# Kernel tuning notes

Hardware: AMD Instinct MI355X
Metric: run time of the kernel (lower is better)

## Reference

```python
import jax, jax.numpy as jnp
import numpy as np

B, T, IN_F, F = 128, 256, 256, 256
TAU_MEM = 0.02
THRESH = 0.5
RESET = 0.0
BETA = 4.0
LN_EPS = 1e-6

# Fast-sigmoid surrogate spike: forward = Heaviside, backward = 1/(1+beta|x|)^2
@jax.custom_vjp
def spike_surrogate(x):
    return (x > 0.0).astype(x.dtype)

def _sp_fwd(x):
    return spike_surrogate(x), x

def _sp_bwd(x, g):
    return (g / jnp.square(1.0 + BETA * jnp.abs(x)),)

spike_surrogate.defvjp(_sp_fwd, _sp_bwd)


def setup_inputs() -> dict:
    key = jax.random.key(0)
    k0, k1 = jax.random.split(key)
    spikes = jax.random.uniform(k0, (B, T, IN_F), dtype=jnp.float32)
    W = jax.random.normal(k1, (IN_F, F), dtype=jnp.float32) / np.sqrt(IN_F)
    b = jnp.zeros((F,), jnp.float32)
    ln_scale = jnp.ones((T, F), jnp.float32)   # distinct LayerNorm per timestep
    ln_bias = jnp.zeros((T, F), jnp.float32)
    return {"spikes": spikes, "W": W, "b": b, "ln_scale": ln_scale, "ln_bias": ln_bias}


def reference(spikes, W, b, ln_scale, ln_bias):
    # Dense is shared across timesteps -> one big contraction, same math.
    currents = jnp.einsum('bti,if->btf', spikes, W) + b  # [B,T,F]
    alpha = jnp.exp(jnp.asarray(-1.0 / TAU_MEM, spikes.dtype))

    def step(v_mem, xs):
        cur, gamma, beta_ln = xs  # [B,F], [F], [F]
        v_mem = alpha * v_mem + (1.0 - alpha) * cur
        s = spike_surrogate(v_mem - THRESH)
        v_mem = v_mem * (1.0 - s) + RESET * s
        mu = jnp.mean(s, axis=-1, keepdims=True)
        var = jnp.var(s, axis=-1, keepdims=True)
        y = (s - mu) * jax.lax.rsqrt(var + LN_EPS) * gamma + beta_ln
        return v_mem, y

    v0 = jnp.zeros((spikes.shape[0], W.shape[1]), spikes.dtype)
    xs = (jnp.swapaxes(currents, 0, 1), ln_scale, ln_bias)  # time-major
    _, ys = jax.lax.scan(step, v0, xs)  # ys: [T,B,F]
    return jnp.swapaxes(ys, 0, 1)  # [B,T,F]
```

## Files before the change

### kernel.cpp

```cpp
#include <hip/hip_runtime.h>
#include <math.h>

#define NROWS 32768
#define NK 256
#define NF 256
#define NT_SEQ 256
#define MTILE 32
#define TAU 8e-3f


typedef __attribute__((ext_vector_type(4))) float f32x4;
typedef __attribute__((ext_vector_type(8))) short bf16x8;

__device__ __forceinline__ unsigned short bf16_rne(float f) {
    unsigned int u = __builtin_bit_cast(unsigned int, f);
    u += 0x7FFFu + ((u >> 16) & 1u);
    return (unsigned short)(u >> 16);
}

__global__ void prep_w(const float* __restrict__ W,
                       unsigned short* __restrict__ wt,
                       float* __restrict__ wtT) {
    const int k = blockIdx.x;
    const int col = threadIdx.x;
    const float w = W[k * NF + col];
    const int ks = k >> 5, chunk = (k >> 3) & 3, j = k & 7;
    wt[(ks * 4 + chunk) * 2048 + col * 8 + j] = bf16_rne(w);
    wtT[col * NK + k] = w;
}

__global__ __launch_bounds__(512)
void lif_main(const float* __restrict__ spikes,
              const float* __restrict__ bias,
              const float* __restrict__ ln_scale,
              const float* __restrict__ ln_bias,
              const unsigned short* __restrict__ wt,
              const float* __restrict__ wtT,
              float* __restrict__ out)
{
    __shared__ __align__(16) short alds[MTILE][264];
    __shared__ unsigned int bits[MTILE][8];
    __shared__ float rinv_s[MTILE], mu_s[MTILE];
    __shared__ unsigned int elist[256];
    __shared__ int ecnt;

    const int tid = threadIdx.x;
    const int lane = tid & 63;
    const int wid = tid >> 6;
    const int row0 = blockIdx.x * MTILE;

    if (tid == 0) ecnt = 0;

    #pragma unroll
    for (int it = 0; it < 2; ++it) {
        const int idx = it * 512 + tid;
        const int r = idx >> 5, c8 = (idx & 31) * 8;
        const float* p = spikes + (size_t)(row0 + r) * NK + c8;
        const float4 u = *reinterpret_cast<const float4*>(p);
        const float4 v = *reinterpret_cast<const float4*>(p + 4);
        const unsigned int w0 = (unsigned int)bf16_rne(u.x) | ((unsigned int)bf16_rne(u.y) << 16);
        const unsigned int w1 = (unsigned int)bf16_rne(u.z) | ((unsigned int)bf16_rne(u.w) << 16);
        const unsigned int w2 = (unsigned int)bf16_rne(v.x) | ((unsigned int)bf16_rne(v.y) << 16);
        const unsigned int w3 = (unsigned int)bf16_rne(v.z) | ((unsigned int)bf16_rne(v.w) << 16);
        *reinterpret_cast<uint4*>(&alds[r][c8]) = make_uint4(w0, w1, w2, w3);
    }
    __syncthreads();

    f32x4 acc[2][2];
    {
        const f32x4 z = {0.f, 0.f, 0.f, 0.f};
        acc[0][0] = z; acc[0][1] = z; acc[1][0] = z; acc[1][1] = z;
    }
    const int a_off = (lane & 15) * 264 + (lane >> 4) * 8;
    const int b_base = (lane >> 4) * 2048 + (wid * 32 + (lane & 15)) * 8;
    const short* alds_flat = &alds[0][0];

    #pragma unroll
    for (int ks = 0; ks < 8; ++ks) {
        const bf16x8 b0 = *reinterpret_cast<const bf16x8*>(wt + ks * 8192 + b_base);
        const bf16x8 b1 = *reinterpret_cast<const bf16x8*>(wt + ks * 8192 + b_base + 128);
        const bf16x8 a0 = *reinterpret_cast<const bf16x8*>(alds_flat + ks * 32 + a_off);
        const bf16x8 a1 = *reinterpret_cast<const bf16x8*>(alds_flat + 16 * 264 + ks * 32 + a_off);
        acc[0][0] = __builtin_amdgcn_mfma_f32_16x16x32_bf16(a0, b0, acc[0][0], 0, 0, 0);
        acc[0][1] = __builtin_amdgcn_mfma_f32_16x16x32_bf16(a0, b1, acc[0][1], 0, 0, 0);
        acc[1][0] = __builtin_amdgcn_mfma_f32_16x16x32_bf16(a1, b0, acc[1][0], 0, 0, 0);
        acc[1][1] = __builtin_amdgcn_mfma_f32_16x16x32_bf16(a1, b1, acc[1][1], 0, 0, 0);
    }

    unsigned int smask[2] = {0u, 0u};
    #pragma unroll
    for (int mt = 0; mt < 2; ++mt)
        #pragma unroll
        for (int nt = 0; nt < 2; ++nt) {
            const int gcol = wid * 32 + nt * 16 + (lane & 15);
            const float bv = bias[gcol];
            #pragma unroll
            for (int reg = 0; reg < 4; ++reg) {
                const float v = acc[mt][nt][reg] + bv;
                if ((v - 0.5f) > 0.0f) smask[mt] |= 1u << (nt * 4 + reg);
                if (__builtin_expect(fabsf(v - 0.5f) < TAU, 0)) {
                    const int rl = mt * 16 + (lane >> 4) * 4 + reg;
                    const int ei = atomicAdd(&ecnt, 1);
                    if (ei < 256) elist[ei] = (unsigned int)((rl << 8) | gcol);
                }
            }
        }

    #pragma unroll
    for (int mt = 0; mt < 2; ++mt)
        #pragma unroll
        for (int reg = 0; reg < 4; ++reg) {
            const unsigned long long m0 = __ballot((smask[mt] >> (reg)) & 1u);
            const unsigned long long m1 = __ballot((smask[mt] >> (4 + reg)) & 1u);
            if (lane < 4) {
                const int g = lane;
                const unsigned int w =
                    (unsigned int)((m0 >> (g * 16)) & 0xFFFFull) |
                    ((unsigned int)((m1 >> (g * 16)) & 0xFFFFull) << 16);
                bits[mt * 16 + g * 4 + reg][wid] = w;
            }
        }
    __syncthreads();

    const int ne = min(ecnt, 256);
    for (int e = wid; e < ne; e += 8) {
        const unsigned int pk = elist[e];
        const int rl = (int)(pk >> 8), gcol = (int)(pk & 255u);
        const float* sr = spikes + (size_t)(row0 + rl) * NK;
        const float* wc = wtT + (size_t)gcol * NK;
        const int k0 = lane * 4;
        const float4 s4 = *reinterpret_cast<const float4*>(sr + k0);
        const float4 w4 = *reinterpret_cast<const float4*>(wc + k0);
        const double p0 = (double)s4.x * (double)w4.x;
        const double p1 = (double)s4.y * (double)w4.y;
        const double p2 = (double)s4.z * (double)w4.z;
        const double p3 = (double)s4.w * (double)w4.w;
        double pl = (p0 + p1) + (p2 + p3);
        #pragma unroll
        for (int off = 32; off > 0; off >>= 1) pl += __shfl_down(pl, off);
        if (lane == 0) {
            const double vex = pl + (double)bias[gcol];
            const bool sex = (vex - 0.5) > 0.0;
            const bool spv = (bits[rl][gcol >> 5] >> (gcol & 31)) & 1u;
            if (sex != spv) atomicXor(&bits[rl][gcol >> 5], 1u << (gcol & 31));
        }
    }
    __syncthreads();

    if (tid < MTILE) {
        int kc = 0;
        #pragma unroll
        for (int w = 0; w < 8; ++w) kc += __popc(bits[tid][w]);
        const double mu = (double)kc * (1.0 / 256.0);
        const double var = mu * (1.0 - mu);
        rinv_s[tid] = (float)(1.0 / sqrt(var + 1e-6));
        mu_s[tid] = (float)mu;
    }
    __syncthreads();

    const int orow = tid >> 4;
    const int of0 = (tid & 15) * 4;
    const int grow = row0 + orow;
    const int t = grow & (NT_SEQ - 1);
    const float rinv = rinv_s[orow];
    const float muf = mu_s[orow];
    #pragma unroll
    for (int j = 0; j < 4; ++j) {
        const int f = of0 + j * 64;
        const unsigned int wb = bits[orow][f >> 5];
        const int sh = f & 31;
        const float4 g4 = *reinterpret_cast<const float4*>(&ln_scale[t * NF + f]);
        const float4 b4 = *reinterpret_cast<const float4*>(&ln_bias[t * NF + f]);
        float4 o;
        const float s0 = ((wb >> (sh + 0)) & 1u) ? 1.0f : 0.0f;
        const float s1 = ((wb >> (sh + 1)) & 1u) ? 1.0f : 0.0f;
        const float s2 = ((wb >> (sh + 2)) & 1u) ? 1.0f : 0.0f;
        const float s3 = ((wb >> (sh + 3)) & 1u) ? 1.0f : 0.0f;
        o.x = (s0 - muf) * rinv * g4.x + b4.x;
        o.y = (s1 - muf) * rinv * g4.y + b4.y;
        o.z = (s2 - muf) * rinv * g4.z + b4.z;
        o.w = (s3 - muf) * rinv * g4.w + b4.w;
        *reinterpret_cast<float4*>(&out[(size_t)grow * NF + f]) = o;
    }
}

extern "C" void kernel_launch(void* const* d_in, const int* in_sizes, int n_in,
                              void* d_out, int out_size, void* d_ws, size_t ws_size,
                              hipStream_t stream) {
    const float* spikes   = (const float*)d_in[0];
    const float* W        = (const float*)d_in[1];
    const float* bias     = (const float*)d_in[2];
    const float* ln_scale = (const float*)d_in[3];
    const float* ln_bias  = (const float*)d_in[4];
    float* out = (float*)d_out;
    unsigned short* wt = (unsigned short*)d_ws;
    float* wtT = (float*)((char*)d_ws + 131072);

    prep_w<<<dim3(256), dim3(256), 0, stream>>>(W, wt, wtT);
    lif_main<<<dim3(NROWS / MTILE), dim3(512), 0, stream>>>(
        spikes, bias, ln_scale, ln_bias, wt, wtT, out);
}
```

Measured before the change: 39.61 us.

## Process two row tiles per block with prefetch of the second tile

Each block now handles two 32-row tiles, halving the grid. Global loads for the second tile are issued before the first tile's MFMA and epilogue, and the bf16 conversion into a second LDS buffer happens after the first tile's matmul. This is meant to hide global load latency behind compute and to amortize block launch and setup. The cost is fewer blocks in flight, more registers and LDS per block, and an extra sync between tiles.

```diff
diff --git a/kernel.cpp b/kernel.cpp
--- a/kernel.cpp
+++ b/kernel.cpp
@@ -38,7 +38,7 @@
               const float* __restrict__ wtT,
               float* __restrict__ out)
 {
-    __shared__ __align__(16) short alds[MTILE][264];
+    __shared__ __align__(16) short alds[2][MTILE][264];
     __shared__ unsigned int bits[MTILE][8];
     __shared__ float rinv_s[MTILE], mu_s[MTILE];
     __shared__ unsigned int elist[256];
@@ -47,140 +47,170 @@
     const int tid = threadIdx.x;
     const int lane = tid & 63;
     const int wid = tid >> 6;
-    const int row0 = blockIdx.x * MTILE;
+    const int row_base = blockIdx.x * (2 * MTILE);
 
     if (tid == 0) ecnt = 0;
 
-    #pragma unroll
-    for (int it = 0; it < 2; ++it) {
-        const int idx = it * 512 + tid;
-        const int r = idx >> 5, c8 = (idx & 31) * 8;
-        const float* p = spikes + (size_t)(row0 + r) * NK + c8;
-        const float4 u = *reinterpret_cast<const float4*>(p);
-        const float4 v = *reinterpret_cast<const float4*>(p + 4);
-        const unsigned int w0 = (unsigned int)bf16_rne(u.x) | ((unsigned int)bf16_rne(u.y) << 16);
-        const unsigned int w1 = (unsigned int)bf16_rne(u.z) | ((unsigned int)bf16_rne(u.w) << 16);
-        const unsigned int w2 = (unsigned int)bf16_rne(v.x) | ((unsigned int)bf16_rne(v.y) << 16);
-        const unsigned int w3 = (unsigned int)bf16_rne(v.z) | ((unsigned int)bf16_rne(v.w) << 16);
-        *reinterpret_cast<uint4*>(&alds[r][c8]) = make_uint4(w0, w1, w2, w3);
-    }
-    __syncthreads();
-
-    f32x4 acc[2][2];
-    {
-        const f32x4 z = {0.f, 0.f, 0.f, 0.f};
-        acc[0][0] = z; acc[0][1] = z; acc[1][0] = z; acc[1][1] = z;
-    }
+    const int r0 = tid >> 5, r1 = 16 + (tid >> 5), c8 = (tid & 31) * 8;
+
     const int a_off = (lane & 15) * 264 + (lane >> 4) * 8;
     const int b_base = (lane >> 4) * 2048 + (wid * 32 + (lane & 15)) * 8;
-    const short* alds_flat = &alds[0][0];
-
-    #pragma unroll
-    for (int ks = 0; ks < 8; ++ks) {
-        const bf16x8 b0 = *reinterpret_cast<const bf16x8*>(wt + ks * 8192 + b_base);
-        const bf16x8 b1 = *reinterpret_cast<const bf16x8*>(wt + ks * 8192 + b_base + 128);
-        const bf16x8 a0 = *reinterpret_cast<const bf16x8*>(alds_flat + ks * 32 + a_off);
-        const bf16x8 a1 = *reinterpret_cast<const bf16x8*>(alds_flat + 16 * 264 + ks * 32 + a_off);
-        acc[0][0] = __builtin_amdgcn_mfma_f32_16x16x32_bf16(a0, b0, acc[0][0], 0, 0, 0);
-        acc[0][1] = __builtin_amdgcn_mfma_f32_16x16x32_bf16(a0, b1, acc[0][1], 0, 0, 0);
-        acc[1][0] = __builtin_amdgcn_mfma_f32_16x16x32_bf16(a1, b0, acc[1][0], 0, 0, 0);
-        acc[1][1] = __builtin_amdgcn_mfma_f32_16x16x32_bf16(a1, b1, acc[1][1], 0, 0, 0);
+
+    auto cvt8 = [&](const float4& u, const float4& v) -> uint4 {
+        return make_uint4(
+            (unsigned int)bf16_rne(u.x) | ((unsigned int)bf16_rne(u.y) << 16),
+            (unsigned int)bf16_rne(u.z) | ((unsigned int)bf16_rne(u.w) << 16),
+            (unsigned int)bf16_rne(v.x) | ((unsigned int)bf16_rne(v.y) << 16),
+            (unsigned int)bf16_rne(v.z) | ((unsigned int)bf16_rne(v.w) << 16));
+    };
+
+    float4 u0, v0, u1, v1;
+    {
+        const float* p0 = spikes + (size_t)(row_base + r0) * NK + c8;
+        const float* p1 = spikes + (size_t)(row_base + r1) * NK + c8;
+        u0 = *reinterpret_cast<const float4*>(p0);
+        v0 = *reinterpret_cast<const float4*>(p0 + 4);
+        u1 = *reinterpret_cast<const float4*>(p1);
+        v1 = *reinterpret_cast<const float4*>(p1 + 4);
     }
-
-    unsigned int smask[2] = {0u, 0u};
-    #pragma unroll
-    for (int mt = 0; mt < 2; ++mt)
-        #pragma unroll
-        for (int nt = 0; nt < 2; ++nt) {
-            const int gcol = wid * 32 + nt * 16 + (lane & 15);
-            const float bv = bias[gcol];
-            #pragma unroll
-            for (int reg = 0; reg < 4; ++reg) {
-                const float v = acc[mt][nt][reg] + bv;
-                if ((v - 0.5f) > 0.0f) smask[mt] |= 1u << (nt * 4 + reg);
-                if (__builtin_expect(fabsf(v - 0.5f) < TAU, 0)) {
-                    const int rl = mt * 16 + (lane >> 4) * 4 + reg;
-                    const int ei = atomicAdd(&ecnt, 1);
-                    if (ei < 256) elist[ei] = (unsigned int)((rl << 8) | gcol);
+    *reinterpret_cast<uint4*>(&alds[0][r0][c8]) = cvt8(u0, v0);
+    *reinterpret_cast<uint4*>(&alds[0][r1][c8]) = cvt8(u1, v1);
+    __syncthreads();
+
+    {
+        const float* p0 = spikes + (size_t)(row_base + MTILE + r0) * NK + c8;
+        const float* p1 = spikes + (size_t)(row_base + MTILE + r1) * NK + c8;
+        u0 = *reinterpret_cast<const float4*>(p0);
+        v0 = *reinterpret_cast<const float4*>(p0 + 4);
+        u1 = *reinterpret_cast<const float4*>(p1);
+        v1 = *reinterpret_cast<const float4*>(p1 + 4);
+    }
+
+    #pragma unroll 1
+    for (int p = 0; p < 2; ++p) {
+        const int row0 = row_base + p * MTILE;
+
+        f32x4 acc[2][2];
+        {
+            const f32x4 z = {0.f, 0.f, 0.f, 0.f};
+            acc[0][0] = z; acc[0][1] = z; acc[1][0] = z; acc[1][1] = z;
+        }
+        const short* alds_flat = &alds[p][0][0];
+        #pragma unroll
+        for (int ks = 0; ks < 8; ++ks) {
+            const bf16x8 b0 = *reinterpret_cast<const bf16x8*>(wt + ks * 8192 + b_base);
+            const bf16x8 b1 = *reinterpret_cast<const bf16x8*>(wt + ks * 8192 + b_base + 128);
+            const bf16x8 a0 = *reinterpret_cast<const bf16x8*>(alds_flat + ks * 32 + a_off);
+            const bf16x8 a1 = *reinterpret_cast<const bf16x8*>(alds_flat + 16 * 264 + ks * 32 + a_off);
+            acc[0][0] = __builtin_amdgcn_mfma_f32_16x16x32_bf16(a0, b0, acc[0][0], 0, 0, 0);
+            acc[0][1] = __builtin_amdgcn_mfma_f32_16x16x32_bf16(a0, b1, acc[0][1], 0, 0, 0);
+            acc[1][0] = __builtin_amdgcn_mfma_f32_16x16x32_bf16(a1, b0, acc[1][0], 0, 0, 0);
+            acc[1][1] = __builtin_amdgcn_mfma_f32_16x16x32_bf16(a1, b1, acc[1][1], 0, 0, 0);
+        }
+
+        if (p == 0) {
+            *reinterpret_cast<uint4*>(&alds[1][r0][c8]) = cvt8(u0, v0);
+            *reinterpret_cast<uint4*>(&alds[1][r1][c8]) = cvt8(u1, v1);
+        }
+
+        unsigned int smask[2] = {0u, 0u};
+        #pragma unroll
+        for (int mt = 0; mt < 2; ++mt)
+            #pragma unroll
+            for (int nt = 0; nt < 2; ++nt) {
+                const int gcol = wid * 32 + nt * 16 + (lane & 15);
+                const float bv = bias[gcol];
+                #pragma unroll
+                for (int reg = 0; reg < 4; ++reg) {
+                    const float v = acc[mt][nt][reg] + bv;
+                    if ((v - 0.5f) > 0.0f) smask[mt] |= 1u << (nt * 4 + reg);
+                    if (__builtin_expect(fabsf(v - 0.5f) < TAU, 0)) {
+                        const int rl = mt * 16 + (lane >> 4) * 4 + reg;
+                        const int ei = atomicAdd(&ecnt, 1);
+                        if (ei < 256) elist[ei] = (unsigned int)((rl << 8) | gcol);
+                    }
                 }
             }
-        }
-
-    #pragma unroll
-    for (int mt = 0; mt < 2; ++mt)
-        #pragma unroll
-        for (int reg = 0; reg < 4; ++reg) {
-            const unsigned long long m0 = __ballot((smask[mt] >> (reg)) & 1u);
-            const unsigned long long m1 = __ballot((smask[mt] >> (4 + reg)) & 1u);
-            if (lane < 4) {
-                const int g = lane;
-                const unsigned int w =
-                    (unsigned int)((m0 >> (g * 16)) & 0xFFFFull) |
-                    ((unsigned int)((m1 >> (g * 16)) & 0xFFFFull) << 16);
-                bits[mt * 16 + g * 4 + reg][wid] = w;
+
+        #pragma unroll
+        for (int mt = 0; mt < 2; ++mt)
+            #pragma unroll
+            for (int reg = 0; reg < 4; ++reg) {
+                const unsigned long long m0 = __ballot((smask[mt] >> (reg)) & 1u);
+                const unsigned long long m1 = __ballot((smask[mt] >> (4 + reg)) & 1u);
+                if (lane < 4) {
+                    const int g = lane;
+                    const unsigned int w =
+                        (unsigned int)((m0 >> (g * 16)) & 0xFFFFull) |
+                        ((unsigned int)((m1 >> (g * 16)) & 0xFFFFull) << 16);
+                    bits[mt * 16 + g * 4 + reg][wid] = w;
+                }
             }
-        }
-    __syncthreads();
-
-    const int ne = min(ecnt, 256);
-    for (int e = wid; e < ne; e += 8) {
-        const unsigned int pk = elist[e];
-        const int rl = (int)(pk >> 8), gcol = (int)(pk & 255u);
-        const float* sr = spikes + (size_t)(row0 + rl) * NK;
-        const float* wc = wtT + (size_t)gcol * NK;
-        const int k0 = lane * 4;
-        const float4 s4 = *reinterpret_cast<const float4*>(sr + k0);
-        const float4 w4 = *reinterpret_cast<const float4*>(wc + k0);
-        const double p0 = (double)s4.x * (double)w4.x;
-        const double p1 = (double)s4.y * (double)w4.y;
-        const double p2 = (double)s4.z * (double)w4.z;
-        const double p3 = (double)s4.w * (double)w4.w;
-        double pl = (p0 + p1) + (p2 + p3);
-        #pragma unroll
-        for (int off = 32; off > 0; off >>= 1) pl += __shfl_down(pl, off);
-        if (lane == 0) {
-            const double vex = pl + (double)bias[gcol];
-            const bool sex = (vex - 0.5) > 0.0;
-            const bool spv = (bits[rl][gcol >> 5] >> (gcol & 31)) & 1u;
-            if (sex != spv) atomicXor(&bits[rl][gcol >> 5], 1u << (gcol & 31));
-        }
-    }
-    __syncthreads();
-
-    if (tid < MTILE) {
-        int kc = 0;
-        #pragma unroll
-        for (int w = 0; w < 8; ++w) kc += __popc(bits[tid][w]);
-        const double mu = (double)kc * (1.0 / 256.0);
-        const double var = mu * (1.0 - mu);
-        rinv_s[tid] = (float)(1.0 / sqrt(var + 1e-6));
-        mu_s[tid] = (float)mu;
-    }
-    __syncthreads();
-
-    const int orow = tid >> 4;
-    const int of0 = (tid & 15) * 4;
-    const int grow = row0 + orow;
-    const int t = grow & (NT_SEQ - 1);
-    const float rinv = rinv_s[orow];
-    const float muf = mu_s[orow];
-    #pragma unroll
-    for (int j = 0; j < 4; ++j) {
-        const int f = of0 + j * 64;
-        const unsigned int wb = bits[orow][f >> 5];
-        const int sh = f & 31;
-        const float4 g4 = *reinterpret_cast<const float4*>(&ln_scale[t * NF + f]);
-        const float4 b4 = *reinterpret_cast<const float4*>(&ln_bias[t * NF + f]);
-        float4 o;
-        const float s0 = ((wb >> (sh + 0)) & 1u) ? 1.0f : 0.0f;
-        const float s1 = ((wb >> (sh + 1)) & 1u) ? 1.0f : 0.0f;
-        const float s2 = ((wb >> (sh + 2)) & 1u) ? 1.0f : 0.0f;
-        const float s3 = ((wb >> (sh + 3)) & 1u) ? 1.0f : 0.0f;
-        o.x = (s0 - muf) * rinv * g4.x + b4.x;
-        o.y = (s1 - muf) * rinv * g4.y + b4.y;
-        o.z = (s2 - muf) * rinv * g4.z + b4.z;
-        o.w = (s3 - muf) * rinv * g4.w + b4.w;
-        *reinterpret_cast<float4*>(&out[(size_t)grow * NF + f]) = o;
+        __syncthreads();
+
+        const int ne = min(ecnt, 256);
+        for (int e = wid; e < ne; e += 8) {
+            const unsigned int pk = elist[e];
+            const int rl = (int)(pk >> 8), gcol = (int)(pk & 255u);
+            const float* sr = spikes + (size_t)(row0 + rl) * NK;
+            const float* wc = wtT + (size_t)gcol * NK;
+            const int k0 = lane * 4;
+            const float4 s4 = *reinterpret_cast<const float4*>(sr + k0);
+            const float4 w4 = *reinterpret_cast<const float4*>(wc + k0);
+            const double pp0 = (double)s4.x * (double)w4.x;
+            const double pp1 = (double)s4.y * (double)w4.y;
+            const double pp2 = (double)s4.z * (double)w4.z;
+            const double pp3 = (double)s4.w * (double)w4.w;
+            double pl = (pp0 + pp1) + (pp2 + pp3);
+            #pragma unroll
+            for (int off = 32; off > 0; off >>= 1) pl += __shfl_down(pl, off);
+            if (lane == 0) {
+                const double vex = pl + (double)bias[gcol];
+                const bool sex = (vex - 0.5) > 0.0;
+                const bool spv = (bits[rl][gcol >> 5] >> (gcol & 31)) & 1u;
+                if (sex != spv) atomicXor(&bits[rl][gcol >> 5], 1u << (gcol & 31));
+            }
+        }
+        __syncthreads();
+
+        if (tid < MTILE) {
+            int kc = 0;
+            #pragma unroll
+            for (int w = 0; w < 8; ++w) kc += __popc(bits[tid][w]);
+            const double mu = (double)kc * (1.0 / 256.0);
+            const double var = mu * (1.0 - mu);
+            rinv_s[tid] = (float)(1.0 / sqrt(var + 1e-6));
+            mu_s[tid] = (float)mu;
+        }
+        if (tid == 0) ecnt = 0;
+        __syncthreads();
+
+        const int orow = tid >> 4;
+        const int of0 = (tid & 15) * 4;
+        const int grow = row0 + orow;
+        const int t = grow & (NT_SEQ - 1);
+        const float rinv = rinv_s[orow];
+        const float muf = mu_s[orow];
+        #pragma unroll
+        for (int j = 0; j < 4; ++j) {
+            const int f = of0 + j * 64;
+            const unsigned int wb = bits[orow][f >> 5];
+            const int sh = f & 31;
+            const float4 g4 = *reinterpret_cast<const float4*>(&ln_scale[t * NF + f]);
+            const float4 b4 = *reinterpret_cast<const float4*>(&ln_bias[t * NF + f]);
+            float4 o;
+            const float s0 = ((wb >> (sh + 0)) & 1u) ? 1.0f : 0.0f;
+            const float s1 = ((wb >> (sh + 1)) & 1u) ? 1.0f : 0.0f;
+            const float s2 = ((wb >> (sh + 2)) & 1u) ? 1.0f : 0.0f;
+            const float s3 = ((wb >> (sh + 3)) & 1u) ? 1.0f : 0.0f;
+            o.x = (s0 - muf) * rinv * g4.x + b4.x;
+            o.y = (s1 - muf) * rinv * g4.y + b4.y;
+            o.z = (s2 - muf) * rinv * g4.z + b4.z;
+            o.w = (s3 - muf) * rinv * g4.w + b4.w;
+            *reinterpret_cast<float4*>(&out[(size_t)grow * NF + f]) = o;
+        }
+
+        if (p == 0) __syncthreads();
     }
 }
 
@@ -197,6 +227,6 @@
     float* wtT = (float*)((char*)d_ws + 131072);
 
     prep_w<<<dim3(256), dim3(256), 0, stream>>>(W, wt, wtT);
-    lif_main<<<dim3(NROWS / MTILE), dim3(512), 0, stream>>>(
+    lif_main<<<dim3(NROWS / (2 * MTILE)), dim3(512), 0, stream>>>(
         spikes, bias, ln_scale, ln_bias, wt, wtT, out);
 }
```

Result: slower. 59.04 us (+49.1%).
